# Kernel tuning notes

Measured on AMD Instinct MI355X. Metric: run time of the kernel, lower is better.

The kernel has to match this reference:

```python
import jax, jax.numpy as jnp
import numpy as np

B, N = 2, 4096
BN_EPS = 1e-5
INV_STD = np.float32(1.0 / np.sqrt(1.0 + BN_EPS))  # BN inference: running_mean=0, running_var=1


def pconv(x, w):
    # 1x1 Conv1d == per-point matmul: x [B,C,N], w [Cout,Cin] -> [B,Cout,N]
    return jnp.einsum('oc,bcn->bon', w, x)


def bn(x, g, b):
    # inference BatchNorm1d with mean=0, var=1
    return x * (INV_STD * g)[None, :, None] + b[None, :, None]


def sa_layer(x, qk_w, v_w, v_b, t_w, t_b, g, b):
    # PCT offset-attention. q_conv and k_conv share weights, so energy is a Gram matrix.
    xq = pconv(x, qk_w)                                   # [B, C//2, N]
    energy = jnp.einsum('bcn,bcm->bnm', xq, xq)           # [B, N, N]
    att = jax.nn.softmax(energy, axis=-1)
    att = att / (1e-9 + att.sum(axis=1, keepdims=True))   # extra L1 renorm over dim=1
    xv = pconv(x, v_w) + v_b[None, :, None]               # [B, C, N]
    x_r = jnp.einsum('bcn,bnm->bcm', xv, att)             # [B, C, N]
    # offset=True branch
    x_r = jax.nn.relu(bn(pconv(x - x_r, t_w) + t_b[None, :, None], g, b))
    return x + x_r


def _forward(x, conv1_w, bn1_g, bn1_b, conv2_w, bn2_g, bn2_b, conv3_w, bn3_g, bn3_b,
             pt1_w, pt1_g, pt1_b, pt2_w, pt2_g, pt2_b,
             sa1_qk, sa1_vw, sa1_vb, sa1_tw, sa1_tb, sa1_g, sa1_b,
             sa2_qk, sa2_vw, sa2_vb, sa2_tw, sa2_tb, sa2_g, sa2_b,
             cf_w, cf_g, cf_b, s1_w, s1_g, s1_b, s2_w, s2_g, s2_b, s3_w):
    h = jnp.transpose(x, (0, 2, 1))                       # [B, 3, N]
    h = jax.nn.relu(bn(pconv(h, conv1_w), bn1_g, bn1_b))  # [B, 64, N]
    h = jax.nn.relu(bn(pconv(h, conv2_w), bn2_g, bn2_b))  # [B, 128, N]
    h = jax.nn.relu(bn(pconv(h, conv3_w), bn3_g, bn3_b))  # [B, 256, N]
    # Point_Transformer_Last
    h = jax.nn.relu(bn(pconv(h, pt1_w), pt1_g, pt1_b))
    h = jax.nn.relu(bn(pconv(h, pt2_w), pt2_g, pt2_b))
    x1 = sa_layer(h, sa1_qk, sa1_vw, sa1_vb, sa1_tw, sa1_tb, sa1_g, sa1_b)
    x2 = sa_layer(x1, sa2_qk, sa2_vw, sa2_vb, sa2_tw, sa2_tb, sa2_g, sa2_b)
    # original forward reuses sa2's weights for layers 3 and 4
    x3 = sa_layer(x2, sa2_qk, sa2_vw, sa2_vb, sa2_tw, sa2_tb, sa2_g, sa2_b)
    x4 = sa_layer(x3, sa2_qk, sa2_vw, sa2_vb, sa2_tw, sa2_tb, sa2_g, sa2_b)
    h = jnp.concatenate([x1, x2, x3, x4], axis=1)         # [B, 1024, N]
    face = jax.nn.leaky_relu(bn(pconv(h, cf_w), cf_g, cf_b), 0.2)  # [B, 512, N]
    gmax = jnp.max(face, axis=2, keepdims=True)           # adaptive_max_pool1d(.,1)
    h = jnp.concatenate([face, jnp.broadcast_to(gmax, face.shape)], axis=1)  # [B, 1024, N]
    h = jax.nn.leaky_relu(bn(pconv(h, s1_w), s1_g, s1_b), 0.2)
    h = jax.nn.leaky_relu(bn(pconv(h, s2_w), s2_g, s2_b), 0.2)
    h = pconv(h, s3_w)                                    # [B, 50, N]
    return jnp.transpose(h, (0, 2, 1))                    # [B, N, 50]


def setup_inputs() -> dict:
    key = jax.random.key(0)
    kit = iter(jax.random.split(key, 80))
    def W(co, ci):
        return jax.random.normal(next(kit), (co, ci), dtype=jnp.float32) / np.float32(np.sqrt(ci))
    def G(c):
        return 1.0 + 0.1 * jax.random.normal(next(kit), (c,), dtype=jnp.float32)
    def Bv(c):
        return 0.1 * jax.random.normal(next(kit), (c,), dtype=jnp.float32)
    d = {}
    d['x'] = jax.random.normal(next(kit), (B, N, 3), dtype=jnp.float32)
    d['conv1_w'] = W(64, 3);   d['bn1_g'] = G(64);  d['bn1_b'] = Bv(64)
    d['conv2_w'] = W(128, 64); d['bn2_g'] = G(128); d['bn2_b'] = Bv(128)
    d['conv3_w'] = W(256, 128); d['bn3_g'] = G(256); d['bn3_b'] = Bv(256)
    d['pt1_w'] = W(256, 256); d['pt1_g'] = G(256); d['pt1_b'] = Bv(256)
    d['pt2_w'] = W(256, 256); d['pt2_g'] = G(256); d['pt2_b'] = Bv(256)
    for p in ('sa1', 'sa2'):
        d[p + '_qk'] = 0.1 * W(128, 256)  # small scale keeps softmax unsaturated
        d[p + '_vw'] = W(256, 256); d[p + '_vb'] = Bv(256)
        d[p + '_tw'] = W(256, 256); d[p + '_tb'] = Bv(256)
        d[p + '_g'] = G(256); d[p + '_b'] = Bv(256)
    d['cf_w'] = W(512, 1024); d['cf_g'] = G(512); d['cf_b'] = Bv(512)
    d['s1_w'] = W(512, 1024); d['s1_g'] = G(512); d['s1_b'] = Bv(512)
    d['s2_w'] = W(256, 512); d['s2_g'] = G(256); d['s2_b'] = Bv(256)
    d['s3_w'] = W(50, 256)
    return d


def reference(x, conv1_w, bn1_g, bn1_b, conv2_w, bn2_g, bn2_b, conv3_w, bn3_g, bn3_b,
              pt1_w, pt1_g, pt1_b, pt2_w, pt2_g, pt2_b,
              sa1_qk, sa1_vw, sa1_vb, sa1_tw, sa1_tb, sa1_g, sa1_b,
              sa2_qk, sa2_vw, sa2_vb, sa2_tw, sa2_tb, sa2_g, sa2_b,
              cf_w, cf_g, cf_b, s1_w, s1_g, s1_b, s2_w, s2_g, s2_b, s3_w):
    return _forward(x, conv1_w, bn1_g, bn1_b, conv2_w, bn2_g, bn2_b, conv3_w, bn3_g, bn3_b,
                    pt1_w, pt1_g, pt1_b, pt2_w, pt2_g, pt2_b,
                    sa1_qk, sa1_vw, sa1_vb, sa1_tw, sa1_tb, sa1_g, sa1_b,
                    sa2_qk, sa2_vw, sa2_vb, sa2_tw, sa2_tb, sa2_g, sa2_b,
                    cf_w, cf_g, cf_b, s1_w, s1_g, s1_b, s2_w, s2_g, s2_b, s3_w)
```

## Files before the change

### kernel.cpp

```cpp
#include <hip/hip_runtime.h>
#include <hip/hip_bf16.h>


#define NPTS 4096
#define BATCH 2
#define MSPLIT 4
#define RSSPLIT 8
static constexpr float INV_STD = 0.9999950000374997f;

__device__ __forceinline__ float bf2f(unsigned short u) {
    return __uint_as_float(((unsigned int)u) << 16);
}
__device__ __forceinline__ unsigned short f2bf(float f) {
    unsigned int x = __float_as_uint(f);
    unsigned int r = (x + 0x7FFFu + ((x >> 16) & 1u)) >> 16;
    return (unsigned short)r;
}

__device__ __forceinline__ void async16(const unsigned short* g, unsigned short* l)
{
    __builtin_amdgcn_global_load_lds(
        (const __attribute__((address_space(1))) unsigned int*)(const void*)g,
        (__attribute__((address_space(3))) unsigned int*)(void*)l,
        16, 0, 0);
}

typedef __attribute__((ext_vector_type(8))) short short8;
typedef __attribute__((ext_vector_type(4))) float f32x4;

struct WSplit {
    const float* src[14];
    int n[14];
    long long off[14];
};

__global__ __launch_bounds__(256)
void presplit_k(WSplit d, unsigned short* __restrict__ wbuf)
{
    int wi = blockIdx.y;
    int i = blockIdx.x * 256 + threadIdx.x;
    int n = d.n[wi];
    if (i >= n) return;
    float v = d.src[wi][i];
    unsigned short h = f2bf(v);
    unsigned short* dst = wbuf + d.off[wi];
    dst[i] = h;
    dst[n + i] = f2bf(v - bf2f(h));
}

__device__ __forceinline__ void nt_epilogue(
    float y, int rg, int cg, int b, int Nb,
    const float* bias, int bias_mode,
    const float* bng, const float* bnb,
    const unsigned short* res, long long res_bs, int res_ld, long long res_po,
    int act, int out_mode,
    void* Cp, long long c_bs, int c_ld, long long c_po)
{
    if (bias) {
        if (bias_mode == 3)      y += bias[rg];
        else if (bias_mode == 2) y += bias[b * Nb + cg];
        else                     y += bias[cg];
    }
    if (bng) y = y * (INV_STD * bng[cg]) + bnb[cg];
    if (act == 1) y = fmaxf(y, 0.f);
    else if (act == 2) y = (y > 0.f) ? y : 0.2f * y;
    if (res) {
        long long ri_ = (long long)b * res_bs + (long long)rg * res_ld + cg;
        y += bf2f(res[ri_]) + bf2f(res[res_po + ri_]);
    }
    long long ci = (long long)b * c_bs + (long long)rg * c_ld + cg;
    if (out_mode == 0) {
        unsigned short* C = (unsigned short*)Cp;
        unsigned short h = f2bf(y);
        C[ci] = h;
        C[c_po + ci] = f2bf(y - bf2f(h));
    } else if (out_mode == 1) {
        ((unsigned short*)Cp)[ci] = f2bf(y);
    } else {
        if (cg < Nb) ((float*)Cp)[ci] = y;
    }
}

__global__ __launch_bounds__(256)
void gemm_nt_split(const unsigned short* __restrict__ A, long long a_bs, int a_lda, long long a_po,
                   const unsigned short* __restrict__ B, long long b_bs, int b_lda, long long b_po,
                   void* __restrict__ Cp, long long c_bs, int c_ld, long long c_po,
                   int Nb, int K,
                   const float* __restrict__ bias, int bias_mode,
                   const float* __restrict__ bng, const float* __restrict__ bnb,
                   const unsigned short* __restrict__ res, long long res_bs, int res_ld, long long res_po,
                   int act, int out_mode)
{
    __shared__ unsigned short As[2][64 * 64];
    __shared__ unsigned short Bs[2][64 * 64];
    const int b = blockIdx.z;
    const int m0 = blockIdx.y * 64, n0 = blockIdx.x * 64;
    const int t = threadIdx.x;
    const int lane = t & 63, w = t >> 6;
    const int wr = (w >> 1) * 32, wc = (w & 1) * 32;
    const int ml = lane & 15, q = lane >> 4;

    f32x4 acc[2][2] = {};

    for (int k0 = 0; k0 < K; k0 += 64) {
        __syncthreads();
        #pragma unroll
        for (int e = 0; e < 2; e++) {
            int idx = t + e * 256;
            int row = idx >> 3, blk = idx & 7;
            int gblk = blk ^ (row & 7);
            int lofs = (e * 256 + (t & 192)) * 8;
            const unsigned short* sA = A + (long long)b * a_bs
                                     + (long long)(m0 + row) * a_lda + k0 + gblk * 8;
            const unsigned short* sB = B + (long long)b * b_bs
                                     + (long long)(n0 + row) * b_lda + k0 + gblk * 8;
            async16(sA,        &As[0][0] + lofs);
            async16(sA + a_po, &As[1][0] + lofs);
            async16(sB,        &Bs[0][0] + lofs);
            async16(sB + b_po, &Bs[1][0] + lofs);
        }
        __syncthreads();
        #pragma unroll
        for (int kk = 0; kk < 2; kk++) {
            short8 ah[2], al[2], bh[2], bl[2];
            #pragma unroll
            for (int it = 0; it < 2; it++) {
                int row = wr + it * 16 + ml;
                int slot = (kk * 4 + q) ^ (row & 7);
                ah[it] = *(const short8*)(&As[0][row * 64 + slot * 8]);
                al[it] = *(const short8*)(&As[1][row * 64 + slot * 8]);
            }
            #pragma unroll
            for (int jt = 0; jt < 2; jt++) {
                int row = wc + jt * 16 + ml;
                int slot = (kk * 4 + q) ^ (row & 7);
                bh[jt] = *(const short8*)(&Bs[0][row * 64 + slot * 8]);
                bl[jt] = *(const short8*)(&Bs[1][row * 64 + slot * 8]);
            }
            #pragma unroll
            for (int it = 0; it < 2; it++)
                #pragma unroll
                for (int jt = 0; jt < 2; jt++) {
                    acc[it][jt] = __builtin_amdgcn_mfma_f32_16x16x32_bf16(ah[it], bh[jt], acc[it][jt], 0, 0, 0);
                    acc[it][jt] = __builtin_amdgcn_mfma_f32_16x16x32_bf16(ah[it], bl[jt], acc[it][jt], 0, 0, 0);
                    acc[it][jt] = __builtin_amdgcn_mfma_f32_16x16x32_bf16(al[it], bh[jt], acc[it][jt], 0, 0, 0);
                }
        }
    }

    #pragma unroll
    for (int it = 0; it < 2; it++)
        #pragma unroll
        for (int jt = 0; jt < 2; jt++)
            #pragma unroll
            for (int r = 0; r < 4; r++)
                nt_epilogue(acc[it][jt][r], m0 + wr + it * 16 + q * 4 + r,
                            n0 + wc + jt * 16 + ml, b, Nb,
                            bias, bias_mode, bng, bnb, res, res_bs, res_ld, res_po,
                            act, out_mode, Cp, c_bs, c_ld, c_po);
}

__global__ __launch_bounds__(256)
void gemm_nt_splitB(const unsigned short* __restrict__ A, long long a_bs, int a_lda, long long a_po,
                    const unsigned short* __restrict__ B, long long b_bs, int b_lda, long long b_po,
                    void* __restrict__ Cp, long long c_bs, int c_ld, long long c_po,
                    int Nb, int K,
                    const float* __restrict__ bias, int bias_mode,
                    const float* __restrict__ bng, const float* __restrict__ bnb,
                    const unsigned short* __restrict__ res, long long res_bs, int res_ld, long long res_po,
                    int act, int out_mode)
{
    __shared__ unsigned short As[2][2][64 * 64];
    __shared__ unsigned short Bs[2][2][64 * 64];
    const int b = blockIdx.z;
    const int m0 = blockIdx.y * 64, n0 = blockIdx.x * 64;
    const int t = threadIdx.x;
    const int lane = t & 63, w = t >> 6;
    const int wr = (w >> 1) * 32, wc = (w & 1) * 32;
    const int ml = lane & 15, q = lane >> 4;

    f32x4 acc[2][2] = {};

    for (int k0 = 0; k0 < K; k0 += 128) {
        __syncthreads();
        #pragma unroll
        for (int sub = 0; sub < 2; sub++) {
            int kb = k0 + sub * 64;
            #pragma unroll
            for (int e = 0; e < 2; e++) {
                int idx = t + e * 256;
                int row = idx >> 3, blk = idx & 7;
                int gblk = blk ^ (row & 7);
                int lofs = (e * 256 + (t & 192)) * 8;
                const unsigned short* sA = A + (long long)b * a_bs
                                         + (long long)(m0 + row) * a_lda + kb + gblk * 8;
                const unsigned short* sB = B + (long long)b * b_bs
                                         + (long long)(n0 + row) * b_lda + kb + gblk * 8;
                async16(sA,        &As[0][sub][0] + lofs);
                async16(sA + a_po, &As[1][sub][0] + lofs);
                async16(sB,        &Bs[0][sub][0] + lofs);
                async16(sB + b_po, &Bs[1][sub][0] + lofs);
            }
        }
        __syncthreads();
        #pragma unroll
        for (int sub = 0; sub < 2; sub++)
            #pragma unroll
            for (int kk = 0; kk < 2; kk++) {
                short8 ah[2], al[2], bh[2], bl[2];
                #pragma unroll
                for (int it = 0; it < 2; it++) {
                    int row = wr + it * 16 + ml;
                    int slot = (kk * 4 + q) ^ (row & 7);
                    ah[it] = *(const short8*)(&As[0][sub][row * 64 + slot * 8]);
                    al[it] = *(const short8*)(&As[1][sub][row * 64 + slot * 8]);
                }
                #pragma unroll
                for (int jt = 0; jt < 2; jt++) {
                    int row = wc + jt * 16 + ml;
                    int slot = (kk * 4 + q) ^ (row & 7);
                    bh[jt] = *(const short8*)(&Bs[0][sub][row * 64 + slot * 8]);
                    bl[jt] = *(const short8*)(&Bs[1][sub][row * 64 + slot * 8]);
                }
                #pragma unroll
                for (int it = 0; it < 2; it++)
                    #pragma unroll
                    for (int jt = 0; jt < 2; jt++) {
                        acc[it][jt] = __builtin_amdgcn_mfma_f32_16x16x32_bf16(ah[it], bh[jt], acc[it][jt], 0, 0, 0);
                        acc[it][jt] = __builtin_amdgcn_mfma_f32_16x16x32_bf16(ah[it], bl[jt], acc[it][jt], 0, 0, 0);
                        acc[it][jt] = __builtin_amdgcn_mfma_f32_16x16x32_bf16(al[it], bh[jt], acc[it][jt], 0, 0, 0);
                    }
            }
    }

    #pragma unroll
    for (int it = 0; it < 2; it++)
        #pragma unroll
        for (int jt = 0; jt < 2; jt++)
            #pragma unroll
            for (int r = 0; r < 4; r++)
                nt_epilogue(acc[it][jt][r], m0 + wr + it * 16 + q * 4 + r,
                            n0 + wc + jt * 16 + ml, b, Nb,
                            bias, bias_mode, bng, bnb, res, res_bs, res_ld, res_po,
                            act, out_mode, Cp, c_bs, c_ld, c_po);
}

__global__ __launch_bounds__(256)
void rs_k(const unsigned short* __restrict__ xq, float* __restrict__ rs)
{
    __shared__ unsigned short Kq[2][64 * 64];
    const int b = blockIdx.z;
    const int p0 = blockIdx.y * 64;
    const int m_beg = blockIdx.x * (NPTS / RSSPLIT);
    const unsigned short* xqB = xq + (long long)b * NPTS * 128;
    const int t = threadIdx.x;
    const int lane = t & 63, w = t >> 6;
    const int pw = w * 16;
    const int ml = lane & 15, q = lane >> 4;

    short8 af[4];
    #pragma unroll
    for (int ks = 0; ks < 4; ks++)
        af[ks] = *(const short8*)(xqB + (long long)(p0 + pw + ml) * 128 + ks * 32 + q * 8);

    float rsum[4] = {0.f, 0.f, 0.f, 0.f};

    for (int m0 = m_beg; m0 < m_beg + NPTS / RSSPLIT; m0 += 64) {
        __syncthreads();
        #pragma unroll
        for (int e = 0; e < 4; e++) {
            int idx = t + e * 256;
            int sub = idx >> 9, row = (idx >> 3) & 63, blk = idx & 7;
            int gblk = blk ^ (row & 7);
            int lofs = (e * 256 + (t & 192)) * 8;
            async16(xqB + (long long)(m0 + row) * 128 + sub * 64 + gblk * 8,
                    &Kq[0][0] + lofs);
        }
        __syncthreads();
        f32x4 acc[4] = {};
        #pragma unroll
        for (int ks = 0; ks < 4; ks++) {
            int kh = ks >> 1, kk = ks & 1;
            #pragma unroll
            for (int jt = 0; jt < 4; jt++) {
                int row = jt * 16 + ml;
                int slot = (kk * 4 + q) ^ (row & 7);
                short8 bf = *(const short8*)(&Kq[kh][row * 64 + slot * 8]);
                acc[jt] = __builtin_amdgcn_mfma_f32_16x16x32_bf16(af[ks], bf, acc[jt], 0, 0, 0);
            }
        }
        #pragma unroll
        for (int jt = 0; jt < 4; jt++)
            #pragma unroll
            for (int r = 0; r < 4; r++)
                rsum[r] += __expf(acc[jt][r]);
    }
    #pragma unroll
    for (int r = 0; r < 4; r++) {
        float s = rsum[r];
        s += __shfl_xor(s, 1); s += __shfl_xor(s, 2);
        s += __shfl_xor(s, 4); s += __shfl_xor(s, 8);
        if (ml == 0) atomicAdd(&rs[b * NPTS + p0 + pw + q * 4 + r], s);
    }
}

__global__ __launch_bounds__(256)
void attn_pv(const unsigned short* __restrict__ xq,
             const unsigned short* __restrict__ xv,
             const float* __restrict__ rs,
             float* __restrict__ part,
             float* __restrict__ csp)
{
    __shared__ unsigned short Kq[2][64 * 64];
    __shared__ unsigned short Vv[256 * 64];
    __shared__ unsigned short Pl[64][72];
    const int z = blockIdx.z, b = z / MSPLIT, ms = z % MSPLIT;
    const int p0 = blockIdx.y * 64;
    const unsigned short* xqB = xq + (long long)b * NPTS * 128;
    const unsigned short* xvB = xv + (long long)b * 256 * NPTS;
    const float* rsB = rs + b * NPTS;
    const int t = threadIdx.x;
    const int lane = t & 63, w = t >> 6;
    const int pw = w * 16;
    const int cw = w * 64;
    const int ml = lane & 15, q = lane >> 4;

    short8 af[4];
    #pragma unroll
    for (int ks = 0; ks < 4; ks++)
        af[ks] = *(const short8*)(xqB + (long long)(p0 + pw + ml) * 128 + ks * 32 + q * 8);

    f32x4 pv[4][4] = {};
    float csr[4] = {0.f, 0.f, 0.f, 0.f};

    const int m_beg = ms * (NPTS / MSPLIT);
    for (int m0 = m_beg; m0 < m_beg + NPTS / MSPLIT; m0 += 64) {
        __syncthreads();
        #pragma unroll
        for (int e = 0; e < 4; e++) {
            int idx = t + e * 256;
            int sub = idx >> 9, row = (idx >> 3) & 63, blk = idx & 7;
            int gblk = blk ^ (row & 7);
            int lofs = (e * 256 + (t & 192)) * 8;
            async16(xqB + (long long)(m0 + row) * 128 + sub * 64 + gblk * 8,
                    &Kq[0][0] + lofs);
        }
        #pragma unroll
        for (int e = 0; e < 8; e++) {
            int idx = t + e * 256;
            int row = idx >> 3, blk = idx & 7;
            int gblk = blk ^ (row & 7);
            int lofs = (e * 256 + (t & 192)) * 8;
            async16(xvB + (long long)row * NPTS + m0 + gblk * 8, Vv + lofs);
        }
        __syncthreads();
        f32x4 acc[4] = {};
        #pragma unroll
        for (int ks = 0; ks < 4; ks++) {
            int kh = ks >> 1, kk = ks & 1;
            #pragma unroll
            for (int jt = 0; jt < 4; jt++) {
                int row = jt * 16 + ml;
                int slot = (kk * 4 + q) ^ (row & 7);
                short8 bf = *(const short8*)(&Kq[kh][row * 64 + slot * 8]);
                acc[jt] = __builtin_amdgcn_mfma_f32_16x16x32_bf16(af[ks], bf, acc[jt], 0, 0, 0);
            }
        }
        #pragma unroll
        for (int jt = 0; jt < 4; jt++) {
            float rvm = 1.f / rsB[m0 + jt * 16 + ml];
            #pragma unroll
            for (int r = 0; r < 4; r++) {
                float pvv = __expf(acc[jt][r]) * rvm;
                csr[r] += pvv;
                Pl[pw + q * 4 + r][jt * 16 + ml] = f2bf(pvv);
            }
        }
        __syncthreads();
        #pragma unroll
        for (int kk = 0; kk < 2; kk++) {
            short8 ap[4];
            #pragma unroll
            for (int pst = 0; pst < 4; pst++)
                ap[pst] = *(const short8*)(&Pl[pst * 16 + ml][kk * 32 + q * 8]);
            #pragma unroll
            for (int jt = 0; jt < 4; jt++) {
                int row = cw + jt * 16 + ml;
                int slot = (kk * 4 + q) ^ (row & 7);
                short8 bv = *(const short8*)(&Vv[row * 64 + slot * 8]);
                #pragma unroll
                for (int pst = 0; pst < 4; pst++)
                    pv[pst][jt] = __builtin_amdgcn_mfma_f32_16x16x32_bf16(
                        ap[pst], bv, pv[pst][jt], 0, 0, 0);
            }
        }
    }
    #pragma unroll
    for (int r = 0; r < 4; r++) {
        float s = csr[r];
        s += __shfl_xor(s, 1); s += __shfl_xor(s, 2);
        s += __shfl_xor(s, 4); s += __shfl_xor(s, 8);
        if (ml == 0) csp[(long long)z * NPTS + p0 + pw + q * 4 + r] = s;
    }
    float* C = part + (long long)z * ((long long)NPTS * 256);
    #pragma unroll
    for (int pst = 0; pst < 4; pst++)
        #pragma unroll
        for (int jt = 0; jt < 4; jt++)
            #pragma unroll
            for (int r = 0; r < 4; r++) {
                int rg = p0 + pst * 16 + q * 4 + r;
                int cg = cw + jt * 16 + ml;
                C[(long long)rg * 256 + cg] = pv[pst][jt][r];
            }
}

__global__ __launch_bounds__(256)
void conv1_k(const float* __restrict__ x, const float* __restrict__ w,
             const float* __restrict__ g, const float* __restrict__ bb,
             unsigned short* __restrict__ h, long long h_po)
{
    int b = blockIdx.y;
    int p = blockIdx.x * 4 + (threadIdx.x >> 6);
    int c = threadIdx.x & 63;
    const float* xp = x + ((long long)b * NPTS + p) * 3;
    float y = xp[0] * w[c * 3] + xp[1] * w[c * 3 + 1] + xp[2] * w[c * 3 + 2];
    y = y * (INV_STD * g[c]) + bb[c];
    y = fmaxf(y, 0.f);
    long long i = ((long long)b * NPTS + p) * 64 + c;
    unsigned short hi = f2bf(y);
    h[i] = hi;
    h[h_po + i] = f2bf(y - bf2f(hi));
}

__global__ __launch_bounds__(256)
void zero_k(float* __restrict__ p, int n)
{
    int i = blockIdx.x * 256 + threadIdx.x;
    if (i < n) p[i] = 0.f;
}

__global__ __launch_bounds__(256)
void diff_k(const unsigned short* __restrict__ xin, long long x_bs, int x_ld, long long x_po,
            const float* __restrict__ part, const float* __restrict__ csp,
            unsigned short* __restrict__ d, long long d_po)
{
    long long i = (long long)blockIdx.x * 256 + threadIdx.x;
    int b = blockIdx.y;
    int p = (int)(i >> 8), c = (int)(i & 255);
    long long xi = (long long)b * x_bs + (long long)p * x_ld + c;
    float xv = bf2f(xin[xi]) + bf2f(xin[x_po + xi]);
    float xr = 0.f, den = 1e-9f;
    #pragma unroll
    for (int ks = 0; ks < MSPLIT; ks++) {
        int z = b * MSPLIT + ks;
        xr  += part[(long long)z * ((long long)NPTS * 256) + i];
        den += csp[(long long)z * NPTS + p];
    }
    float v = xv - xr / den;
    long long di = (long long)b * NPTS * 256 + i;
    unsigned short hi = f2bf(v);
    d[di] = hi;
    d[d_po + di] = f2bf(v - bf2f(hi));
}

__global__ __launch_bounds__(256)
void gmaxp_k(const unsigned short* __restrict__ face, long long f_po, float* __restrict__ pm)
{
    int c = blockIdx.x * 256 + threadIdx.x;
    int ch = blockIdx.y;
    int b = blockIdx.z;
    float m = -3.4e38f;
    for (int j = 0; j < 256; j++) {
        long long i = ((long long)b * NPTS + ch * 256 + j) * 512 + c;
        m = fmaxf(m, bf2f(face[i]) + bf2f(face[f_po + i]));
    }
    pm[((long long)b * 16 + ch) * 512 + c] = m;
}

__global__ __launch_bounds__(256)
void gmaxr_k(const float* __restrict__ pm, float* __restrict__ gm)
{
    int idx = blockIdx.x * 256 + threadIdx.x;
    int b = idx >> 9, c = idx & 511;
    float m = -3.4e38f;
    for (int ch = 0; ch < 16; ch++)
        m = fmaxf(m, pm[((long long)b * 16 + ch) * 512 + c]);
    gm[idx] = m;
}

__global__ __launch_bounds__(256)
void bias2_k(const float* __restrict__ w, const float* __restrict__ g, float* __restrict__ b2)
{
    int o = blockIdx.x * 256 + threadIdx.x;
    int b = blockIdx.y;
    if (o >= 512) return;
    float s = 0.f;
    for (int c = 0; c < 512; c++) s += w[(long long)o * 1024 + 512 + c] * g[b * 512 + c];
    b2[b * 512 + o] = s;
}

extern "C" void kernel_launch(void* const* d_in, const int* in_sizes, int n_in,
                              void* d_out, int out_size, void* d_ws, size_t ws_size,
                              hipStream_t stream)
{
    const float* x       = (const float*)d_in[0];
    const float* conv1_w = (const float*)d_in[1];
    const float* bn1_g   = (const float*)d_in[2];
    const float* bn1_b   = (const float*)d_in[3];
    const float* conv2_w = (const float*)d_in[4];
    const float* bn2_g   = (const float*)d_in[5];
    const float* bn2_b   = (const float*)d_in[6];
    const float* conv3_w = (const float*)d_in[7];
    const float* bn3_g   = (const float*)d_in[8];
    const float* bn3_b   = (const float*)d_in[9];
    const float* pt1_w   = (const float*)d_in[10];
    const float* pt1_g   = (const float*)d_in[11];
    const float* pt1_b   = (const float*)d_in[12];
    const float* pt2_w   = (const float*)d_in[13];
    const float* pt2_g   = (const float*)d_in[14];
    const float* pt2_b   = (const float*)d_in[15];
    const float* sa_qk[2] = {(const float*)d_in[16], (const float*)d_in[23]};
    const float* sa_vw[2] = {(const float*)d_in[17], (const float*)d_in[24]};
    const float* sa_vb[2] = {(const float*)d_in[18], (const float*)d_in[25]};
    const float* sa_tw[2] = {(const float*)d_in[19], (const float*)d_in[26]};
    const float* sa_tb[2] = {(const float*)d_in[20], (const float*)d_in[27]};
    const float* sa_g[2]  = {(const float*)d_in[21], (const float*)d_in[28]};
    const float* sa_b[2]  = {(const float*)d_in[22], (const float*)d_in[29]};
    const float* cf_w = (const float*)d_in[30];
    const float* cf_g = (const float*)d_in[31];
    const float* cf_b = (const float*)d_in[32];
    const float* s1_w = (const float*)d_in[33];
    const float* s1_g = (const float*)d_in[34];
    const float* s1_b = (const float*)d_in[35];
    const float* s2_w = (const float*)d_in[36];
    const float* s2_g = (const float*)d_in[37];
    const float* s2_b = (const float*)d_in[38];
    const float* s3_w = (const float*)d_in[39];

    char* base = (char*)d_ws;
    size_t off = 0;
    auto alloc = [&](size_t bytes) -> void* {
        void* p = base + off;
        off = (off + bytes + 255) & ~(size_t)255;
        return p;
    };
    const long long N = NPTS;
    const long long PO64   = (long long)BATCH * N * 64;
    const long long PO128  = (long long)BATCH * N * 128;
    const long long PO256  = (long long)BATCH * N * 256;
    const long long PO512  = (long long)BATCH * N * 512;
    const long long PO1024 = (long long)BATCH * N * 1024;

    unsigned short* S1  = (unsigned short*)alloc(2 * PO256 * 2);
    unsigned short* S2  = (unsigned short*)alloc(2 * PO256 * 2);
    unsigned short* Dv  = (unsigned short*)alloc(2 * PO256 * 2);
    unsigned short* cat = (unsigned short*)alloc(2 * PO1024 * 2);
    unsigned short* face = (unsigned short*)alloc(2 * PO512 * 2);
    unsigned short* xq  = (unsigned short*)alloc((size_t)BATCH * N * 128 * 2);
    unsigned short* xv  = (unsigned short*)alloc((size_t)BATCH * 256 * N * 2);
    unsigned short* s1b = (unsigned short*)alloc(2 * PO512 * 2);
    unsigned short* s2b = (unsigned short*)alloc(2 * PO256 * 2);
    float* part = (float*)alloc((size_t)BATCH * MSPLIT * N * 256 * 4);
    float* csp  = (float*)alloc((size_t)BATCH * MSPLIT * N * 4);
    float* rs = (float*)alloc((size_t)BATCH * N * 4);
    float* pm = (float*)alloc((size_t)BATCH * 16 * 512 * 4);
    float* gm = (float*)alloc((size_t)BATCH * 512 * 4);
    float* b2 = (float*)alloc((size_t)BATCH * 512 * 4);
    unsigned short* wb = (unsigned short*)alloc((size_t)3400000 * 2);

    WSplit wd;
    const float* wsrc[14] = {conv2_w, conv3_w, pt1_w, pt2_w, sa_qk[0], sa_qk[1],
                             sa_vw[0], sa_vw[1], sa_tw[0], sa_tw[1], cf_w, s1_w, s2_w, s3_w};
    int wn[14] = {128*64, 256*128, 256*256, 256*256, 128*256, 128*256,
                  256*256, 256*256, 256*256, 256*256, 512*1024, 512*1024, 256*512, 50*256};
    long long wo[14]; long long acc_ = 0;
    for (int i = 0; i < 14; i++) { wd.src[i] = wsrc[i]; wd.n[i] = wn[i]; wd.off[i] = acc_; wo[i] = acc_; acc_ += 2LL * wn[i]; }
    presplit_k<<<dim3((512*1024 + 255) / 256, 14), 256, 0, stream>>>(wd, wb);
    auto W = [&](int i) { return wb + wo[i]; };

    auto nt = [&](const unsigned short* A, long long a_bs, int a_lda, long long a_po,
                  const unsigned short* B, long long b_bs, int b_lda, long long b_po,
                  void* C, long long c_bs, int c_ld, long long c_po,
                  int Mrows, int Nb, int K,
                  const float* bias, int bias_mode,
                  const float* bng, const float* bnb,
                  const unsigned short* res, long long res_bs, int res_ld, long long res_po,
                  int act, int out_mode) {
        dim3 g((Nb + 63) / 64, Mrows / 64, BATCH);
        gemm_nt_split<<<g, 256, 0, stream>>>(A, a_bs, a_lda, a_po, B, b_bs, b_lda, b_po,
                                             C, c_bs, c_ld, c_po, Nb, K,
                                             bias, bias_mode, bng, bnb,
                                             res, res_bs, res_ld, res_po, act, out_mode);
    };
    auto ntB = [&](const unsigned short* A, long long a_bs, int a_lda, long long a_po,
                   const unsigned short* B, long long b_bs, int b_lda, long long b_po,
                   void* C, long long c_bs, int c_ld, long long c_po,
                   int Mrows, int Nb, int K,
                   const float* bias, int bias_mode,
                   const float* bng, const float* bnb,
                   const unsigned short* res, long long res_bs, int res_ld, long long res_po,
                   int act, int out_mode) {
        dim3 g((Nb + 63) / 64, Mrows / 64, BATCH);
        gemm_nt_splitB<<<g, 256, 0, stream>>>(A, a_bs, a_lda, a_po, B, b_bs, b_lda, b_po,
                                              C, c_bs, c_ld, c_po, Nb, K,
                                              bias, bias_mode, bng, bnb,
                                              res, res_bs, res_ld, res_po, act, out_mode);
    };

    conv1_k<<<dim3(NPTS / 4, BATCH), 256, 0, stream>>>(x, conv1_w, bn1_g, bn1_b, S1, PO64);
    nt(S1, N * 64, 64, PO64,    W(0), 0, 64, wn[0],  S2, N * 128, 128, PO128,
       NPTS, 128, 64,  nullptr, 0, bn2_g, bn2_b, nullptr, 0, 0, 0, 1, 0);
    ntB(S2, N * 128, 128, PO128, W(1), 0, 128, wn[1], S1, N * 256, 256, PO256,
        NPTS, 256, 128, nullptr, 0, bn3_g, bn3_b, nullptr, 0, 0, 0, 1, 0);
    ntB(S1, N * 256, 256, PO256, W(2), 0, 256, wn[2], S2, N * 256, 256, PO256,
        NPTS, 256, 256, nullptr, 0, pt1_g, pt1_b, nullptr, 0, 0, 0, 1, 0);
    ntB(S2, N * 256, 256, PO256, W(3), 0, 256, wn[3], S1, N * 256, 256, PO256,
        NPTS, 256, 256, nullptr, 0, pt2_g, pt2_b, nullptr, 0, 0, 0, 1, 0);

    for (int i = 0; i < 4; i++) {
        int p = (i == 0) ? 0 : 1;
        const unsigned short* xin = (i == 0) ? S1 : cat + (size_t)(i - 1) * 256;
        long long xin_bs = (i == 0) ? N * 256 : N * 1024;
        int xin_ld = (i == 0) ? 256 : 1024;
        long long xin_po = (i == 0) ? PO256 : PO1024;

        ntB(xin, xin_bs, xin_ld, xin_po, W(4 + p), 0, 256, wn[4 + p],
            xq, N * 128, 128, 0, NPTS, 128, 256,
            nullptr, 0, nullptr, nullptr, nullptr, 0, 0, 0, 0, 1);
        ntB(W(6 + p), 0, 256, wn[6 + p], xin, xin_bs, xin_ld, xin_po,
            xv, 256 * N, NPTS, 0, 256, NPTS, 256,
            sa_vb[p], 3, nullptr, nullptr, nullptr, 0, 0, 0, 0, 1);
        zero_k<<<(BATCH * NPTS + 255) / 256, 256, 0, stream>>>(rs, BATCH * NPTS);
        rs_k<<<dim3(RSSPLIT, NPTS / 64, BATCH), 256, 0, stream>>>(xq, rs);
        attn_pv<<<dim3(1, NPTS / 64, BATCH * MSPLIT), 256, 0, stream>>>(
            xq, xv, rs, part, csp);
        diff_k<<<dim3(NPTS * 256 / 256, BATCH), 256, 0, stream>>>(
            xin, xin_bs, xin_ld, xin_po, part, csp, Dv, PO256);
        ntB(Dv, N * 256, 256, PO256, W(8 + p), 0, 256, wn[8 + p],
            cat + (size_t)i * 256, N * 1024, 1024, PO1024,
            NPTS, 256, 256, sa_tb[p], 1, sa_g[p], sa_b[p],
            xin, xin_bs, xin_ld, xin_po, 1, 0);
    }

    nt(cat, N * 1024, 1024, PO1024, W(10), 0, 1024, wn[10],
       face, N * 512, 512, PO512, NPTS, 512, 1024,
       nullptr, 0, cf_g, cf_b, nullptr, 0, 0, 0, 2, 0);
    gmaxp_k<<<dim3(2, 16, BATCH), 256, 0, stream>>>(face, PO512, pm);
    gmaxr_k<<<dim3(BATCH * 512 / 256), 256, 0, stream>>>(pm, gm);
    bias2_k<<<dim3(2, BATCH), 256, 0, stream>>>(s1_w, gm, b2);
    nt(face, N * 512, 512, PO512, W(11), 0, 1024, wn[11],
       s1b, N * 512, 512, PO512, NPTS, 512, 512,
       b2, 2, s1_g, s1_b, nullptr, 0, 0, 0, 2, 0);
    ntB(s1b, N * 512, 512, PO512, W(12), 0, 512, wn[12],
        s2b, N * 256, 256, PO256, NPTS, 256, 512,
        nullptr, 0, s2_g, s2_b, nullptr, 0, 0, 0, 2, 0);
    ntB(s2b, N * 256, 256, PO256, W(13), 0, 256, wn[13],
        d_out, N * 50, 50, 0, NPTS, 50, 256,
        nullptr, 0, nullptr, nullptr, nullptr, 0, 0, 0, 0, 2);
}
```

Measured before the change: 786.8 us.

## Double-buffer K tiles and load V fragments directly to registers in attention

Both the row-sum kernel and the attention P·V kernel now double-buffer the K tile in LDS, prefetching the next tile asynchronously while the current one is computed. This drops one barrier per iteration. In attn_pv, the V tile is no longer staged through LDS; each wave loads its V fragments straight from global memory into registers. The P tile is also double-buffered so only one barrier per iteration remains. The aim is to overlap global loads with MFMA work and cut LDS traffic and synchronization, at the cost of more registers and uncoalesced-ish global V reads.

```diff
diff --git a/kernel.cpp b/kernel.cpp
--- a/kernel.cpp
+++ b/kernel.cpp
@@ -248,7 +248,7 @@
 __global__ __launch_bounds__(256)
 void rs_k(const unsigned short* __restrict__ xq, float* __restrict__ rs)
 {
-    __shared__ unsigned short Kq[2][64 * 64];
+    __shared__ unsigned short Kq[2][2][64 * 64];
     const int b = blockIdx.z;
     const int p0 = blockIdx.y * 64;
     const int m_beg = blockIdx.x * (NPTS / RSSPLIT);
@@ -265,8 +265,7 @@
 
     float rsum[4] = {0.f, 0.f, 0.f, 0.f};
 
-    for (int m0 = m_beg; m0 < m_beg + NPTS / RSSPLIT; m0 += 64) {
-        __syncthreads();
+    auto stageK = [&](int m0, int buf) {
         #pragma unroll
         for (int e = 0; e < 4; e++) {
             int idx = t + e * 256;
@@ -274,9 +273,18 @@
             int gblk = blk ^ (row & 7);
             int lofs = (e * 256 + (t & 192)) * 8;
             async16(xqB + (long long)(m0 + row) * 128 + sub * 64 + gblk * 8,
-                    &Kq[0][0] + lofs);
-        }
-        __syncthreads();
+                    &Kq[buf][0][0] + lofs);
+        }
+    };
+
+    constexpr int NIT = (NPTS / RSSPLIT) / 64;
+    stageK(m_beg, 0);
+    __syncthreads();
+
+    for (int it = 0; it < NIT; ++it) {
+        const int m0 = m_beg + it * 64;
+        const int cur = it & 1;
+        if (it + 1 < NIT) stageK(m0 + 64, cur ^ 1);
         f32x4 acc[4] = {};
         #pragma unroll
         for (int ks = 0; ks < 4; ks++) {
@@ -285,7 +293,7 @@
             for (int jt = 0; jt < 4; jt++) {
                 int row = jt * 16 + ml;
                 int slot = (kk * 4 + q) ^ (row & 7);
-                short8 bf = *(const short8*)(&Kq[kh][row * 64 + slot * 8]);
+                short8 bf = *(const short8*)(&Kq[cur][kh][row * 64 + slot * 8]);
                 acc[jt] = __builtin_amdgcn_mfma_f32_16x16x32_bf16(af[ks], bf, acc[jt], 0, 0, 0);
             }
         }
@@ -294,6 +302,7 @@
             #pragma unroll
             for (int r = 0; r < 4; r++)
                 rsum[r] += __expf(acc[jt][r]);
+        __syncthreads();
     }
     #pragma unroll
     for (int r = 0; r < 4; r++) {
@@ -311,9 +320,8 @@
              float* __restrict__ part,
              float* __restrict__ csp)
 {
-    __shared__ unsigned short Kq[2][64 * 64];
-    __shared__ unsigned short Vv[256 * 64];
-    __shared__ unsigned short Pl[64][72];
+    __shared__ unsigned short Kq[2][2][64 * 64];
+    __shared__ unsigned short Pl[2][64][72];
     const int z = blockIdx.z, b = z / MSPLIT, ms = z % MSPLIT;
     const int p0 = blockIdx.y * 64;
     const unsigned short* xqB = xq + (long long)b * NPTS * 128;
@@ -333,9 +341,7 @@
     f32x4 pv[4][4] = {};
     float csr[4] = {0.f, 0.f, 0.f, 0.f};
 
-    const int m_beg = ms * (NPTS / MSPLIT);
-    for (int m0 = m_beg; m0 < m_beg + NPTS / MSPLIT; m0 += 64) {
-        __syncthreads();
+    auto stageK = [&](int m0, int buf) {
         #pragma unroll
         for (int e = 0; e < 4; e++) {
             int idx = t + e * 256;
@@ -343,17 +349,28 @@
             int gblk = blk ^ (row & 7);
             int lofs = (e * 256 + (t & 192)) * 8;
             async16(xqB + (long long)(m0 + row) * 128 + sub * 64 + gblk * 8,
-                    &Kq[0][0] + lofs);
-        }
-        #pragma unroll
-        for (int e = 0; e < 8; e++) {
-            int idx = t + e * 256;
-            int row = idx >> 3, blk = idx & 7;
-            int gblk = blk ^ (row & 7);
-            int lofs = (e * 256 + (t & 192)) * 8;
-            async16(xvB + (long long)row * NPTS + m0 + gblk * 8, Vv + lofs);
-        }
-        __syncthreads();
+                    &Kq[buf][0][0] + lofs);
+        }
+    };
+
+    const int m_beg = ms * (NPTS / MSPLIT);
+    constexpr int NIT = (NPTS / MSPLIT) / 64;
+    stageK(m_beg, 0);
+    __syncthreads();
+
+    for (int it = 0; it < NIT; ++it) {
+        const int m0 = m_beg + it * 64;
+        const int cur = it & 1;
+        if (it + 1 < NIT) stageK(m0 + 64, cur ^ 1);
+        short8 bv[2][4];
+        #pragma unroll
+        for (int kk = 0; kk < 2; kk++)
+            #pragma unroll
+            for (int jt = 0; jt < 4; jt++) {
+                int row = cw + jt * 16 + ml;
+                bv[kk][jt] = *(const short8*)(xvB + (long long)row * NPTS
+                                              + m0 + kk * 32 + q * 8);
+            }
         f32x4 acc[4] = {};
         #pragma unroll
         for (int ks = 0; ks < 4; ks++) {
@@ -362,7 +379,7 @@
             for (int jt = 0; jt < 4; jt++) {
                 int row = jt * 16 + ml;
                 int slot = (kk * 4 + q) ^ (row & 7);
-                short8 bf = *(const short8*)(&Kq[kh][row * 64 + slot * 8]);
+                short8 bf = *(const short8*)(&Kq[cur][kh][row * 64 + slot * 8]);
                 acc[jt] = __builtin_amdgcn_mfma_f32_16x16x32_bf16(af[ks], bf, acc[jt], 0, 0, 0);
             }
         }
@@ -373,7 +390,7 @@
             for (int r = 0; r < 4; r++) {
                 float pvv = __expf(acc[jt][r]) * rvm;
                 csr[r] += pvv;
-                Pl[pw + q * 4 + r][jt * 16 + ml] = f2bf(pvv);
+                Pl[cur][pw + q * 4 + r][jt * 16 + ml] = f2bf(pvv);
             }
         }
         __syncthreads();
@@ -382,17 +399,13 @@
             short8 ap[4];
             #pragma unroll
             for (int pst = 0; pst < 4; pst++)
-                ap[pst] = *(const short8*)(&Pl[pst * 16 + ml][kk * 32 + q * 8]);
-            #pragma unroll
-            for (int jt = 0; jt < 4; jt++) {
-                int row = cw + jt * 16 + ml;
-                int slot = (kk * 4 + q) ^ (row & 7);
-                short8 bv = *(const short8*)(&Vv[row * 64 + slot * 8]);
+                ap[pst] = *(const short8*)(&Pl[cur][pst * 16 + ml][kk * 32 + q * 8]);
+            #pragma unroll
+            for (int jt = 0; jt < 4; jt++)
                 #pragma unroll
                 for (int pst = 0; pst < 4; pst++)
                     pv[pst][jt] = __builtin_amdgcn_mfma_f32_16x16x32_bf16(
-                        ap[pst], bv, pv[pst][jt], 0, 0, 0);
-            }
+                        ap[pst], bv[kk][jt], pv[pst][jt], 0, 0, 0);
         }
     }
     #pragma unroll
```

After: 792.7 us. Within noise of the previous version (+0.8%).
